# Kernel tuning notes

Hardware: AMD Instinct MI355X
Metric: run time of the kernel (lower is better)

## Reference

```python
import jax, jax.numpy as jnp
import numpy as np

N = 100000
E = 600000
IN_DIM = 128
HID = 128


def setup_inputs() -> dict:
    key = jax.random.key(0)
    ks = jax.random.split(key, 12)
    def lin(kw, fan_in, fan_out):
        # torch nn.Linear default init: U(-1/sqrt(fan_in), 1/sqrt(fan_in))
        bound = 1.0 / np.sqrt(fan_in)
        kw1, kw2 = jax.random.split(kw)
        w = jax.random.uniform(kw1, (fan_in, fan_out), jnp.float32, -bound, bound)
        b = jax.random.uniform(kw2, (fan_out,), jnp.float32, -bound, bound)
        return w, b
    x = jax.random.normal(ks[0], (N, IN_DIM), jnp.float32)
    edge_index = jax.random.randint(ks[1], (2, E), 0, N, jnp.int64)
    w1a, b1a = lin(ks[2], IN_DIM, HID)
    w1b, b1b = lin(ks[3], HID, HID)
    w2a, b2a = lin(ks[4], HID, HID)
    w2b, b2b = lin(ks[5], HID, HID)
    wo, bo = lin(ks[6], HID, 1)
    return {"x": x, "edge_index": edge_index,
            "w1a": w1a, "b1a": b1a, "w1b": w1b, "b1b": b1b,
            "w2a": w2a, "b2a": b2a, "w2b": w2b, "b2b": b2b,
            "wo": wo, "bo": bo}


def _gin_conv(x, src, dst, wa, ba, wb, bb):
    # sum-aggregate neighbor features: agg[dst] += x[src]; eps = 0 (GIN default)
    agg = jax.ops.segment_sum(x[src], dst, num_segments=N)
    h = x + agg
    h = jax.nn.relu(h @ wa + ba)
    return h @ wb + bb


def reference(x, edge_index, w1a, b1a, w1b, b1b, w2a, b2a, w2b, b2b, wo, bo):
    src, dst = edge_index[0], edge_index[1]
    h = _gin_conv(x, src, dst, w1a, b1a, w1b, b1b)
    h = _gin_conv(h, src, dst, w2a, b2a, w2b, b2b)
    return (h @ wo + bo).squeeze(-1)  # [N]
```

## Files before the change

### kernel.cpp

```cpp
#include <hip/hip_runtime.h>

typedef unsigned short u16;
typedef unsigned int u32;
typedef __bf16 bf16x8 __attribute__((ext_vector_type(8)));
typedef float f32x4 __attribute__((ext_vector_type(4)));

#define CAP 32

__device__ __forceinline__ u16 f2bf(float f) {
  union { float f; u32 u; } c; c.f = f;
  return (u16)((c.u + 0x7fffu + ((c.u >> 16) & 1u)) >> 16);
}
__device__ __forceinline__ float2 upk2(u32 v) {
  union { u32 u; float f; } a, b; a.u = v << 16; b.u = v & 0xffff0000u;
  return make_float2(a.f, b.f);
}
__device__ __forceinline__ u32 pk2(float x, float y) {
  return (u32)f2bf(x) | ((u32)f2bf(y) << 16);
}

__global__ __launch_bounds__(256) void k_prep2(const float4* __restrict__ x4,
                                               uint2* __restrict__ xb,
                                               int n4, int castBlocks,
                                               const float* __restrict__ w0,
                                               const float* __restrict__ w1,
                                               const float* __restrict__ w2,
                                               const float* __restrict__ w3,
                                               u16* __restrict__ wT) {
  int b = blockIdx.x, t = threadIdx.x;
  if (b < castBlocks) {
    int i = b * 256 + t;
    if (i < n4) {
      float4 v = x4[i];
      xb[i] = make_uint2(pk2(v.x, v.y), pk2(v.z, v.w));
    }
  } else {
    int id = (b - castBlocks) * 256 + t;
    int w = id >> 14, rem = id & 16383;
    int nn = rem >> 7, kk = rem & 127;
    const float* s = (w == 0) ? w0 : (w == 1) ? w1 : (w == 2) ? w2 : w3;
    wT[id] = f2bf(s[kk * 128 + nn]);
  }
}

__global__ __launch_bounds__(256) void k_fillp(const int* __restrict__ src,
                                               const int* __restrict__ dst,
                                               int* __restrict__ cursor,
                                               int* __restrict__ edge_src, int E) {
  int e = blockIdx.x * 256 + threadIdx.x;
  if (e < E) {
    int d = dst[e];
    int pos = atomicAdd(&cursor[d], 1);
    if (pos < CAP) edge_src[d * CAP + pos] = src[e];
  }
}

__global__ __launch_bounds__(256) void k_agg(const uint4* __restrict__ in,
                                             uint4* __restrict__ out,
                                             const int* __restrict__ cursor,
                                             const int* __restrict__ edge_src, int N) {
  int node = __builtin_amdgcn_readfirstlane(blockIdx.x * 4 + (threadIdx.x >> 6));
  if (node >= N) return;
  int lane = threadIdx.x & 63;
  int g = lane >> 4, l = lane & 15;

  float acc[8];
#pragma unroll
  for (int i = 0; i < 8; ++i) acc[i] = 0.f;

  auto fma8 = [&](uint4 v, float w) {
    float2 p;
    p = upk2(v.x); acc[0] = fmaf(w, p.x, acc[0]); acc[1] = fmaf(w, p.y, acc[1]);
    p = upk2(v.y); acc[2] = fmaf(w, p.x, acc[2]); acc[3] = fmaf(w, p.y, acc[3]);
    p = upk2(v.z); acc[4] = fmaf(w, p.x, acc[4]); acc[5] = fmaf(w, p.y, acc[5]);
    p = upk2(v.w); acc[6] = fmaf(w, p.x, acc[6]); acc[7] = fmaf(w, p.y, acc[7]);
  };

  int cnt = cursor[node];
  cnt = (cnt < CAP) ? cnt : CAP;
  int e0 = node * CAP, e1 = e0 + cnt;
  uint4 sv = in[(size_t)node * 16 + l];
  fma8(sv, (g == 0) ? 1.f : 0.f);

  for (int e = e0; e < e1; e += 8) {
    int ea = e + g, eb = e + 4 + g;
    int ca = (ea < e1) ? ea : (e1 - 1);
    int cb = (eb < e1) ? eb : (e1 - 1);
    float wa = (ea < e1) ? 1.f : 0.f;
    float wb = (eb < e1) ? 1.f : 0.f;
    int ia = edge_src[ca];
    int ib = edge_src[cb];
    uint4 va = in[(size_t)ia * 16 + l];
    uint4 vb = in[(size_t)ib * 16 + l];
    fma8(va, wa);
    fma8(vb, wb);
  }

#pragma unroll
  for (int i = 0; i < 8; ++i) {
    acc[i] += __shfl_xor(acc[i], 16, 64);
    acc[i] += __shfl_xor(acc[i], 32, 64);
  }
  if (g == 0) {
    uint4 o;
    o.x = pk2(acc[0], acc[1]);
    o.y = pk2(acc[2], acc[3]);
    o.z = pk2(acc[4], acc[5]);
    o.w = pk2(acc[6], acc[7]);
    out[(size_t)node * 16 + l] = o;
  }
}

template <bool HEAD>
__global__ __launch_bounds__(256) void k_mlp(const u16* __restrict__ in,
                                             const u16* __restrict__ wAT,
                                             const float* __restrict__ bA,
                                             const u16* __restrict__ wBT,
                                             const float* __restrict__ bB,
                                             const float* __restrict__ wo,
                                             const float* __restrict__ bo,
                                             void* __restrict__ outp,
                                             int N, int ntiles) {
  __shared__ u16 lA[64 * 128];
  __shared__ u16 lW[2 * 128 * 128];
  const int tid = threadIdx.x;
  const int wave = tid >> 6, lane = tid & 63;
  const int m16 = lane & 15, quad = lane >> 4;

#pragma unroll
  for (int it = 0; it < 16; ++it) {
    int id = it * 256 + tid;
    int m = id >> 11, rem = id & 2047;
    int row = rem >> 4, c = rem & 15;
    const u16* s = m ? wBT : wAT;
    uint4 v = *(const uint4*)&s[row * 128 + c * 8];
    *(uint4*)&lW[m * 16384 + row * 128 + ((c ^ (row & 15)) << 3)] = v;
  }

  float bAr[8], bBr[8], woR[8], bBh[8];
#pragma unroll
  for (int t = 0; t < 8; ++t) {
    bAr[t] = bA[t * 16 + m16];
    bBr[t] = HEAD ? 0.f : bB[t * 16 + m16];
    woR[t] = HEAD ? wo[t * 16 + m16] : 0.f;
    bBh[t] = HEAD ? bB[t * 16 + m16] : 0.f;
  }
  float boV = HEAD ? bo[0] : 0.f;

  __syncthreads();

  const int mrow = wave * 16 + m16;

  uint4 pf[4];
  auto gload = [&](int tl) {
#pragma unroll
    for (int it = 0; it < 4; ++it) {
      int gr = tl * 64 + wave * 16 + it * 4 + quad;
      uint4 v = make_uint4(0u, 0u, 0u, 0u);
      if (gr < N) v = *(const uint4*)&in[(size_t)gr * 128 + m16 * 8];
      pf[it] = v;
    }
  };

  int tile = blockIdx.x;
  if (tile < ntiles) gload(tile);
  for (; tile < ntiles; tile += gridDim.x) {
#pragma unroll
    for (int it = 0; it < 4; ++it) {
      int row = wave * 16 + it * 4 + quad;
      *(uint4*)&lA[row * 128 + ((m16 ^ (row & 15)) << 3)] = pf[it];
    }
    bf16x8 aF[4];
#pragma unroll
    for (int ks = 0; ks < 4; ++ks)
      aF[ks] = *(const bf16x8*)&lA[mrow * 128 + (((ks * 4 + quad) ^ m16) << 3)];
    int nxt = tile + gridDim.x;
    if (nxt < ntiles) gload(nxt);

    f32x4 acc[8];
#pragma unroll
    for (int t = 0; t < 8; ++t) acc[t] = (f32x4){0.f, 0.f, 0.f, 0.f};
#pragma unroll
    for (int t = 0; t < 8; ++t) {
      int nrow = t * 16 + m16;
#pragma unroll
      for (int ks = 0; ks < 4; ++ks) {
        bf16x8 bF = *(const bf16x8*)&lW[nrow * 128 + (((ks * 4 + quad) ^ m16) << 3)];
        acc[t] = __builtin_amdgcn_mfma_f32_16x16x32_bf16(aF[ks], bF, acc[t], 0, 0, 0);
      }
    }
#pragma unroll
    for (int t = 0; t < 8; ++t) {
      int n = t * 16 + m16;
#pragma unroll
      for (int r = 0; r < 4; ++r) {
        int rloc = quad * 4 + r;
        int absrow = wave * 16 + rloc;
        float v = acc[t][r] + bAr[t];
        v = v > 0.f ? v : 0.f;
        lA[absrow * 128 + ((((n >> 3) ^ rloc) << 3) | (n & 7))] = f2bf(v);
      }
    }
#pragma unroll
    for (int ks = 0; ks < 4; ++ks)
      aF[ks] = *(const bf16x8*)&lA[mrow * 128 + (((ks * 4 + quad) ^ m16) << 3)];
#pragma unroll
    for (int t = 0; t < 8; ++t) acc[t] = (f32x4){0.f, 0.f, 0.f, 0.f};
#pragma unroll
    for (int t = 0; t < 8; ++t) {
      int nrow = t * 16 + m16;
#pragma unroll
      for (int ks = 0; ks < 4; ++ks) {
        bf16x8 bF = *(const bf16x8*)&lW[16384 + nrow * 128 + (((ks * 4 + quad) ^ m16) << 3)];
        acc[t] = __builtin_amdgcn_mfma_f32_16x16x32_bf16(aF[ks], bF, acc[t], 0, 0, 0);
      }
    }
    if (!HEAD) {
#pragma unroll
      for (int t = 0; t < 8; ++t) {
        int n = t * 16 + m16;
#pragma unroll
        for (int r = 0; r < 4; ++r) {
          int rloc = quad * 4 + r;
          int absrow = wave * 16 + rloc;
          float v = acc[t][r] + bBr[t];
          lA[absrow * 128 + ((((n >> 3) ^ rloc) << 3) | (n & 7))] = f2bf(v);
        }
      }
      u16* out = (u16*)outp;
#pragma unroll
      for (int it = 0; it < 4; ++it) {
        int row = wave * 16 + it * 4 + quad;
        int gr = tile * 64 + row;
        if (gr < N) {
          uint4 v = *(const uint4*)&lA[row * 128 + ((m16 ^ (row & 15)) << 3)];
          *(uint4*)&out[(size_t)gr * 128 + m16 * 8] = v;
        }
      }
    } else {
      float* out = (float*)outp;
      float s[4];
#pragma unroll
      for (int r = 0; r < 4; ++r) {
        float v = 0.f;
#pragma unroll
        for (int t = 0; t < 8; ++t) v += (acc[t][r] + bBh[t]) * woR[t];
        s[r] = v;
      }
#pragma unroll
      for (int r = 0; r < 4; ++r) {
        s[r] += __shfl_xor(s[r], 1, 64);
        s[r] += __shfl_xor(s[r], 2, 64);
        s[r] += __shfl_xor(s[r], 4, 64);
        s[r] += __shfl_xor(s[r], 8, 64);
      }
      if (m16 == 0) {
#pragma unroll
        for (int r = 0; r < 4; ++r) {
          int gr = tile * 64 + wave * 16 + quad * 4 + r;
          if (gr < N) out[gr] = s[r] + boV;
        }
      }
    }
  }
}

extern "C" void kernel_launch(void* const* d_in, const int* in_sizes, int n_in,
                              void* d_out, int out_size, void* d_ws, size_t ws_size,
                              hipStream_t stream) {
  const float* x = (const float*)d_in[0];
  const int* ei = (const int*)d_in[1];
  const int E = in_sizes[1] / 2;
  const int N = in_sizes[0] / 128;
  const int* srcI = ei;
  const int* dstI = ei + E;
  const float* w1a = (const float*)d_in[2];
  const float* b1a = (const float*)d_in[3];
  const float* w1b = (const float*)d_in[4];
  const float* b1b = (const float*)d_in[5];
  const float* w2a = (const float*)d_in[6];
  const float* b2a = (const float*)d_in[7];
  const float* w2b = (const float*)d_in[8];
  const float* b2b = (const float*)d_in[9];
  const float* wo = (const float*)d_in[10];
  const float* bo = (const float*)d_in[11];

  char* ws = (char*)d_ws;
  size_t off = 0;
  auto nx = [&](size_t bytes) {
    size_t o = off;
    off += (bytes + 511) & ~(size_t)511;
    return o;
  };
  int* cursor   = (int*)(ws + nx((size_t)N * 4));
  int* edge_src = (int*)(ws + nx((size_t)N * CAP * 4));
  u16* wT       = (u16*)(ws + nx((size_t)4 * 16384 * 2));
  u16* xb       = (u16*)(ws + nx((size_t)N * 128 * 2));
  u16* bufA     = (u16*)(ws + nx((size_t)N * 128 * 2));
  u16* bufB     = (u16*)(ws + nx((size_t)N * 128 * 2));

  const int n4 = N * 32;
  const int castBlocks = (n4 + 255) / 256;
  const int trBlocks = 256;

  hipMemsetAsync(cursor, 0, (size_t)N * 4, stream);
  k_prep2<<<castBlocks + trBlocks, 256, 0, stream>>>(
      (const float4*)x, (uint2*)xb, n4, castBlocks, w1a, w1b, w2a, w2b, wT);
  k_fillp<<<(E + 255) / 256, 256, 0, stream>>>(srcI, dstI, cursor, edge_src, E);

  const int aggBlocks = (N + 3) / 4;
  const int ntiles = (N + 63) / 64;
  const int mlpGrid = 512;

  k_agg<<<aggBlocks, 256, 0, stream>>>((const uint4*)xb, (uint4*)bufA, cursor, edge_src, N);
  k_mlp<false><<<mlpGrid, 256, 0, stream>>>(bufA, wT, b1a, wT + 16384, b1b,
                                            nullptr, nullptr, bufB, N, ntiles);
  k_agg<<<aggBlocks, 256, 0, stream>>>((const uint4*)bufB, (uint4*)xb, cursor, edge_src, N);
  k_mlp<true><<<mlpGrid, 256, 0, stream>>>(xb, wT + 32768, b2a, wT + 49152, b2b,
                                           wo, bo, d_out, N, ntiles);
}
```

Measured before the change: 241.1 us.

## Fold cursor zeroing into prep, halve MLP LDS, pack aggregation FMAs

The cursor memset is folded into the prep kernel as extra zeroing blocks, which removes one launch. The MLP kernel keeps only the first weight matrix in LDS and reads the second matrix's fragments straight from global memory (L2-resident), halving LDS use so more blocks fit per CU, and the MLP grid grows from 512 to 768. The aggregation accumulators become float2 vectors so the compiler can emit packed FMA instructions. The risk is extra global-load latency inside the second GEMM loop.

```diff
diff --git a/kernel.cpp b/kernel.cpp
--- a/kernel.cpp
+++ b/kernel.cpp
@@ -4,6 +4,7 @@
 typedef unsigned int u32;
 typedef __bf16 bf16x8 __attribute__((ext_vector_type(8)));
 typedef float f32x4 __attribute__((ext_vector_type(4)));
+typedef float f32x2 __attribute__((ext_vector_type(2)));
 
 #define CAP 32
 
@@ -15,18 +16,23 @@
   union { u32 u; float f; } a, b; a.u = v << 16; b.u = v & 0xffff0000u;
   return make_float2(a.f, b.f);
 }
+__device__ __forceinline__ f32x2 upk2v(u32 v) {
+  union { u32 u; float f; } a, b; a.u = v << 16; b.u = v & 0xffff0000u;
+  return (f32x2){a.f, b.f};
+}
 __device__ __forceinline__ u32 pk2(float x, float y) {
   return (u32)f2bf(x) | ((u32)f2bf(y) << 16);
 }
 
 __global__ __launch_bounds__(256) void k_prep2(const float4* __restrict__ x4,
                                                uint2* __restrict__ xb,
-                                               int n4, int castBlocks,
+                                               int n4, int castBlocks, int trBlocks,
                                                const float* __restrict__ w0,
                                                const float* __restrict__ w1,
                                                const float* __restrict__ w2,
                                                const float* __restrict__ w3,
-                                               u16* __restrict__ wT) {
+                                               u16* __restrict__ wT,
+                                               int* __restrict__ cursor, int N) {
   int b = blockIdx.x, t = threadIdx.x;
   if (b < castBlocks) {
     int i = b * 256 + t;
@@ -34,12 +40,15 @@
       float4 v = x4[i];
       xb[i] = make_uint2(pk2(v.x, v.y), pk2(v.z, v.w));
     }
-  } else {
+  } else if (b < castBlocks + trBlocks) {
     int id = (b - castBlocks) * 256 + t;
     int w = id >> 14, rem = id & 16383;
     int nn = rem >> 7, kk = rem & 127;
     const float* s = (w == 0) ? w0 : (w == 1) ? w1 : (w == 2) ? w2 : w3;
     wT[id] = f2bf(s[kk * 128 + nn]);
+  } else {
+    int i = (b - castBlocks - trBlocks) * 256 + t;
+    if (i < N) cursor[i] = 0;
   }
 }
 
@@ -64,16 +73,15 @@
   int lane = threadIdx.x & 63;
   int g = lane >> 4, l = lane & 15;
 
-  float acc[8];
-#pragma unroll
-  for (int i = 0; i < 8; ++i) acc[i] = 0.f;
+  f32x2 acc[4];
+#pragma unroll
+  for (int i = 0; i < 4; ++i) acc[i] = (f32x2){0.f, 0.f};
 
   auto fma8 = [&](uint4 v, float w) {
-    float2 p;
-    p = upk2(v.x); acc[0] = fmaf(w, p.x, acc[0]); acc[1] = fmaf(w, p.y, acc[1]);
-    p = upk2(v.y); acc[2] = fmaf(w, p.x, acc[2]); acc[3] = fmaf(w, p.y, acc[3]);
-    p = upk2(v.z); acc[4] = fmaf(w, p.x, acc[4]); acc[5] = fmaf(w, p.y, acc[5]);
-    p = upk2(v.w); acc[6] = fmaf(w, p.x, acc[6]); acc[7] = fmaf(w, p.y, acc[7]);
+    acc[0] += upk2v(v.x) * w;
+    acc[1] += upk2v(v.y) * w;
+    acc[2] += upk2v(v.z) * w;
+    acc[3] += upk2v(v.w) * w;
   };
 
   int cnt = cursor[node];
@@ -96,17 +104,18 @@
     fma8(vb, wb);
   }
 
+  float* af = (float*)acc;
 #pragma unroll
   for (int i = 0; i < 8; ++i) {
-    acc[i] += __shfl_xor(acc[i], 16, 64);
-    acc[i] += __shfl_xor(acc[i], 32, 64);
+    af[i] += __shfl_xor(af[i], 16, 64);
+    af[i] += __shfl_xor(af[i], 32, 64);
   }
   if (g == 0) {
     uint4 o;
-    o.x = pk2(acc[0], acc[1]);
-    o.y = pk2(acc[2], acc[3]);
-    o.z = pk2(acc[4], acc[5]);
-    o.w = pk2(acc[6], acc[7]);
+    o.x = pk2(af[0], af[1]);
+    o.y = pk2(af[2], af[3]);
+    o.z = pk2(af[4], af[5]);
+    o.w = pk2(af[6], af[7]);
     out[(size_t)node * 16 + l] = o;
   }
 }
@@ -122,19 +131,17 @@
                                              void* __restrict__ outp,
                                              int N, int ntiles) {
   __shared__ u16 lA[64 * 128];
-  __shared__ u16 lW[2 * 128 * 128];
+  __shared__ u16 lW[128 * 128];
   const int tid = threadIdx.x;
   const int wave = tid >> 6, lane = tid & 63;
   const int m16 = lane & 15, quad = lane >> 4;
 
 #pragma unroll
-  for (int it = 0; it < 16; ++it) {
+  for (int it = 0; it < 8; ++it) {
     int id = it * 256 + tid;
-    int m = id >> 11, rem = id & 2047;
-    int row = rem >> 4, c = rem & 15;
-    const u16* s = m ? wBT : wAT;
-    uint4 v = *(const uint4*)&s[row * 128 + c * 8];
-    *(uint4*)&lW[m * 16384 + row * 128 + ((c ^ (row & 15)) << 3)] = v;
+    int row = id >> 4, c = id & 15;
+    uint4 v = *(const uint4*)&wAT[row * 128 + c * 8];
+    *(uint4*)&lW[row * 128 + ((c ^ (row & 15)) << 3)] = v;
   }
 
   float bAr[8], bBr[8], woR[8], bBh[8];
@@ -209,11 +216,13 @@
 #pragma unroll
     for (int t = 0; t < 8; ++t) {
       int nrow = t * 16 + m16;
-#pragma unroll
-      for (int ks = 0; ks < 4; ++ks) {
-        bf16x8 bF = *(const bf16x8*)&lW[16384 + nrow * 128 + (((ks * 4 + quad) ^ m16) << 3)];
-        acc[t] = __builtin_amdgcn_mfma_f32_16x16x32_bf16(aF[ks], bF, acc[t], 0, 0, 0);
-      }
+      bf16x8 bG[4];
+#pragma unroll
+      for (int ks = 0; ks < 4; ++ks)
+        bG[ks] = *(const bf16x8*)&wBT[nrow * 128 + (ks * 4 + quad) * 8];
+#pragma unroll
+      for (int ks = 0; ks < 4; ++ks)
+        acc[t] = __builtin_amdgcn_mfma_f32_16x16x32_bf16(aF[ks], bG[ks], acc[t], 0, 0, 0);
     }
     if (!HEAD) {
 #pragma unroll
@@ -302,15 +311,16 @@
   const int n4 = N * 32;
   const int castBlocks = (n4 + 255) / 256;
   const int trBlocks = 256;
-
-  hipMemsetAsync(cursor, 0, (size_t)N * 4, stream);
-  k_prep2<<<castBlocks + trBlocks, 256, 0, stream>>>(
-      (const float4*)x, (uint2*)xb, n4, castBlocks, w1a, w1b, w2a, w2b, wT);
+  const int zeroBlocks = (N + 255) / 256;
+
+  k_prep2<<<castBlocks + trBlocks + zeroBlocks, 256, 0, stream>>>(
+      (const float4*)x, (uint2*)xb, n4, castBlocks, trBlocks,
+      w1a, w1b, w2a, w2b, wT, cursor, N);
   k_fillp<<<(E + 255) / 256, 256, 0, stream>>>(srcI, dstI, cursor, edge_src, E);
 
   const int aggBlocks = (N + 3) / 4;
   const int ntiles = (N + 63) / 64;
-  const int mlpGrid = 512;
+  const int mlpGrid = 768;
 
   k_agg<<<aggBlocks, 256, 0, stream>>>((const uint4*)xb, (uint4*)bufA, cursor, edge_src, N);
   k_mlp<false><<<mlpGrid, 256, 0, stream>>>(bufA, wT, b1a, wT + 16384, b1b,
```

Measured after the change: 256.2 us. 1.06x slower.
